# Performance work log

Measured on AMD Instinct MI355X. Metric: run time of the kernel, lower is better.

The kernel has to match this reference:

```python
import jax, jax.numpy as jnp
import numpy as np

P = 256        # number of graph pairs
LMAX = 32      # max graph size (padded to LMAX+1 incl. virtual node)
F = 2048       # num_input_features
E = 256        # embedding_dim
INF = 10000.0


def _lengths():
    i = np.arange(P)
    len_s = 8 + (i % 25)
    len_t = 8 + ((7 * i + 3) % 25)
    return len_s.astype(np.int32), len_t.astype(np.int32)


def setup_inputs() -> dict:
    key = jax.random.key(0)
    ks = jax.random.split(key, 6)
    len_s_np, len_t_np = _lengths()
    Ns, Nt = int(len_s_np.sum()), int(len_t_np.sum())
    x_s = jax.random.normal(ks[0], (Ns, F), jnp.float32)
    x_t = jax.random.normal(ks[1], (Nt, F), jnp.float32)
    W1 = jax.random.normal(ks[2], (E, F), jnp.float32) / np.float32(np.sqrt(F))
    b1 = jnp.zeros((E,), jnp.float32)
    W2 = jax.random.normal(ks[3], (E, E), jnp.float32) / np.float32(np.sqrt(E))
    b2 = jnp.zeros((E,), jnp.float32)
    virtual_embedding = jax.random.uniform(ks[4], (F,), jnp.float32)
    return {"x_s": x_s, "x_t": x_t, "W1": W1, "b1": b1, "W2": W2, "b2": b2,
            "virtual_embedding": virtual_embedding,
            "len_s": jnp.asarray(len_s_np), "len_t": jnp.asarray(len_t_np)}


def _embed(x, W1, b1, W2, b2):
    # nn.Sequential(Linear, Dropout(eval=identity), ReLU, Linear, ReLU)
    h = jax.nn.relu(x @ W1.T + b1)
    return jax.nn.relu(h @ W2.T + b2)


def _safe_cdist(a, b):
    # a: [P,L,E], b: [P,L,E] -> [P,L,L] Euclidean, grad-safe at 0
    sq = (jnp.sum(a * a, -1)[:, :, None] + jnp.sum(b * b, -1)[:, None, :]
          - 2.0 * jnp.einsum('pid,pjd->pij', a, b))
    sq = jnp.maximum(sq, 0.0)
    pos = sq > 0
    return jnp.where(pos, jnp.sqrt(jnp.where(pos, sq, 1.0)), 0.0)


def _pad_embed(emb, virtual_e, lens):
    # ragged [N,E] -> padded [P,LMAX+1,E]; slot lens[p] (and beyond) = virtual
    pos = jnp.arange(LMAX + 1)
    off = jnp.cumsum(lens) - lens                       # exclusive prefix sum
    idx = off[:, None] + jnp.minimum(pos[None, :], lens[:, None] - 1)
    mask = pos[None, :] < lens[:, None]
    return jnp.where(mask[..., None], emb[idx], virtual_e[None, None, :])


def _edit_costs(x_s, x_t, W1, b1, W2, b2, virtual_embedding, len_s, len_t):
    emb_s = _embed(x_s, W1, b1, W2, b2)
    emb_t = _embed(x_t, W1, b1, W2, b2)
    ve = _embed(virtual_embedding[None, :], W1, b1, W2, b2)[0]
    A = _pad_embed(emb_s, ve, len_s)                    # [P,L+1,E]
    B = _pad_embed(emb_t, ve, len_t)
    d = _safe_cdist(A, B)                               # [P,L+1,L+1]
    pos = jnp.arange(LMAX + 1)
    valid = ((pos[None, :, None] <= len_s[:, None, None]) &
             (pos[None, None, :] <= len_t[:, None, None]))
    tot = jnp.sum(jnp.where(valid, d, 0.0), axis=(1, 2))
    scale = (len_s * len_t).astype(d.dtype) / tot
    return jnp.where(valid, d * scale[:, None, None], 0.0), valid


def _lap_jv(C):
    # Jonker-Volgenant / e-maxx Hungarian for square cost matrix; returns col of each row
    C = np.asarray(C, dtype=np.float64)
    n = C.shape[0]
    u = np.zeros(n + 1)
    v = np.zeros(n + 1)
    p = np.zeros(n + 1, dtype=np.int64)
    way = np.zeros(n + 1, dtype=np.int64)
    for i in range(1, n + 1):
        p[0] = i
        j0 = 0
        minv = np.full(n + 1, np.inf)
        used = np.zeros(n + 1, dtype=bool)
        while True:
            used[j0] = True
            i0 = p[j0]
            cur = C[i0 - 1, :] - u[i0] - v[1:]
            upd = (~used[1:]) & (cur < minv[1:])
            minv[1:][upd] = cur[upd]
            way[1:][upd] = j0
            masked = np.where(used[1:], np.inf, minv[1:])
            j1 = int(np.argmin(masked)) + 1
            delta = masked[j1 - 1]
            u[p[used]] += delta
            v[used] -= delta
            minv[1:][~used[1:]] -= delta
            j0 = j1
            if p[j0] == 0:
                break
        while j0:
            j1 = way[j0]
            p[j0] = p[j1]
            j0 = j1
    row_of_col = p[1:] - 1
    col_of_row = np.empty(n, dtype=np.int64)
    col_of_row[row_of_col] = np.arange(n)
    return col_of_row


def _lsape_align(ec, n, m):
    # LSAPE expansion identical to GEDModelHomology.lsape
    N = n + m
    C = np.zeros((N, N))
    C[:n, :m] = ec[:n, :m]
    C[n:, :m] = INF
    C[:n, m:] = INF
    C[np.arange(n, n + m), np.arange(m)] = ec[n, :m]
    C[np.arange(n), np.arange(m, m + n)] = ec[:n, m]
    C[~np.isfinite(C)] = INF
    p = _lap_jv(C)
    q = np.arange(N)
    align = np.zeros((n + 1, m + 1), dtype=np.int32)
    align[np.minimum(q, n), np.minimum(p, m)] = 1
    align[-1, -1] = 0
    return align


def _alignments(costs_np, len_s_np, len_t_np):
    out = np.zeros((costs_np.shape[0], LMAX + 1, LMAX + 1), dtype=np.int32)
    for pr in range(costs_np.shape[0]):
        n, m = int(len_s_np[pr]), int(len_t_np[pr])
        out[pr, :n + 1, :m + 1] = _lsape_align(costs_np[pr, :n + 1, :m + 1], n, m)
    return out


def reference(x_s, x_t, W1, b1, W2, b2, virtual_embedding, len_s, len_t):
    costs, _ = _edit_costs(x_s, x_t, W1, b1, W2, b2, virtual_embedding, len_s, len_t)
    aligns = jnp.asarray(_alignments(np.asarray(costs),
                                     np.asarray(len_s), np.asarray(len_t)))
    geds = (jnp.sum(aligns.astype(costs.dtype) * costs, axis=(1, 2))
            / (len_s + len_t).astype(costs.dtype))
    return aligns, costs, geds
```

## Files before the change

### kernel.cpp

```cpp
#include <hip/hip_runtime.h>
#include <math.h>

#define LMAXP1 33
#define EDIM   256
#define FBIG   3.0e38f

typedef _Float16 half8 __attribute__((ext_vector_type(8)));
typedef float    f32x4 __attribute__((ext_vector_type(4)));

__device__ inline unsigned pk2h(_Float16 a, _Float16 b) {
    union { _Float16 h[2]; unsigned u; } q; q.h[0] = a; q.h[1] = b; return q.u;
}

#define ASTR 20
__global__ __launch_bounds__(256)
void k_gemm_splitk(const float* __restrict__ S0, int n0,
                   const float* __restrict__ S1, int n1,
                   const float* __restrict__ S2,
                   const float* __restrict__ W,
                   float* __restrict__ Part, int Mtot, int K, int kchunk,
                   const float* __restrict__ bias) {
    __shared__ alignas(16) unsigned AsH[128 * ASTR];
    __shared__ alignas(16) unsigned AsL[128 * ASTR];
    __shared__ alignas(16) unsigned BsH[64 * ASTR];
    __shared__ alignas(16) unsigned BsL[64 * ASTR];
    const int tid  = threadIdx.x;
    const int m0   = blockIdx.x * 128, nc0 = blockIdx.y * 64;
    const int ks   = blockIdx.z;
    const int kb   = ks * kchunk;
    const int ke   = (kb + kchunk < K) ? kb + kchunk : K;

    const int sar = tid >> 1;
    const int sak = (tid & 1) << 4;
    const int sbr = tid >> 2;
    const int sbk = (tid & 3) << 3;

    const int gr = m0 + sar;
    const float* srow = nullptr;
    if (gr < n0)            srow = S0 + (size_t)gr * K;
    else if (gr < n0 + n1)  srow = S1 + (size_t)(gr - n0) * K;
    else if (gr < Mtot)     srow = S2;
    const float* wrow = W + (size_t)(nc0 + sbr) * K;

    const int lane = tid & 63, wv = tid >> 6;
    const int wr = (wv & 1) << 6;
    const int wc = (wv >> 1) << 5;
    const int lr = lane & 15, lq = lane >> 4;

    f32x4 acc[4][2] = {};

    for (int k0 = kb; k0 < ke; k0 += 32) {
        {
            float x[16];
            if (srow) {
                const float4 f0 = *(const float4*)(srow + k0 + sak + 0);
                const float4 f1 = *(const float4*)(srow + k0 + sak + 4);
                const float4 f2 = *(const float4*)(srow + k0 + sak + 8);
                const float4 f3 = *(const float4*)(srow + k0 + sak + 12);
                x[0]=f0.x; x[1]=f0.y; x[2]=f0.z; x[3]=f0.w;
                x[4]=f1.x; x[5]=f1.y; x[6]=f1.z; x[7]=f1.w;
                x[8]=f2.x; x[9]=f2.y; x[10]=f2.z; x[11]=f2.w;
                x[12]=f3.x; x[13]=f3.y; x[14]=f3.z; x[15]=f3.w;
            } else {
                #pragma unroll
                for (int j = 0; j < 16; ++j) x[j] = 0.f;
            }
            unsigned uh[8], ul[8];
            #pragma unroll
            for (int j = 0; j < 8; ++j) {
                const _Float16 h0 = (_Float16)x[2*j],   h1 = (_Float16)x[2*j+1];
                const _Float16 l0 = (_Float16)(x[2*j]   - (float)h0);
                const _Float16 l1 = (_Float16)(x[2*j+1] - (float)h1);
                uh[j] = pk2h(h0, h1); ul[j] = pk2h(l0, l1);
            }
            unsigned* ph = AsH + sar * ASTR + (sak >> 1);
            unsigned* pl = AsL + sar * ASTR + (sak >> 1);
            ((uint4*)ph)[0] = make_uint4(uh[0],uh[1],uh[2],uh[3]);
            ((uint4*)ph)[1] = make_uint4(uh[4],uh[5],uh[6],uh[7]);
            ((uint4*)pl)[0] = make_uint4(ul[0],ul[1],ul[2],ul[3]);
            ((uint4*)pl)[1] = make_uint4(ul[4],ul[5],ul[6],ul[7]);
        }
        {
            const float4 f0 = *(const float4*)(wrow + k0 + sbk + 0);
            const float4 f1 = *(const float4*)(wrow + k0 + sbk + 4);
            float y[8] = {f0.x,f0.y,f0.z,f0.w,f1.x,f1.y,f1.z,f1.w};
            unsigned uh[4], ul[4];
            #pragma unroll
            for (int j = 0; j < 4; ++j) {
                const float a0 = y[2*j] * 1024.0f, a1 = y[2*j+1] * 1024.0f;
                const _Float16 h0 = (_Float16)a0, h1 = (_Float16)a1;
                const _Float16 l0 = (_Float16)(a0 - (float)h0);
                const _Float16 l1 = (_Float16)(a1 - (float)h1);
                uh[j] = pk2h(h0, h1); ul[j] = pk2h(l0, l1);
            }
            *(uint4*)(BsH + sbr * ASTR + (sbk >> 1)) = make_uint4(uh[0],uh[1],uh[2],uh[3]);
            *(uint4*)(BsL + sbr * ASTR + (sbk >> 1)) = make_uint4(ul[0],ul[1],ul[2],ul[3]);
        }
        __syncthreads();

        half8 bh[2], bl[2];
        #pragma unroll
        for (int ct = 0; ct < 2; ++ct) {
            const int br = wc + ct * 16 + lr;
            bh[ct] = *(const half8*)((const char*)BsH + br * 80 + lq * 16);
            bl[ct] = *(const half8*)((const char*)BsL + br * 80 + lq * 16);
        }
        #pragma unroll
        for (int rt = 0; rt < 4; ++rt) {
            const int ar = wr + rt * 16 + lr;
            const half8 ah = *(const half8*)((const char*)AsH + ar * 80 + lq * 16);
            const half8 al = *(const half8*)((const char*)AsL + ar * 80 + lq * 16);
            #pragma unroll
            for (int ct = 0; ct < 2; ++ct) {
                acc[rt][ct] = __builtin_amdgcn_mfma_f32_16x16x32_f16(ah, bh[ct], acc[rt][ct], 0, 0, 0);
                acc[rt][ct] = __builtin_amdgcn_mfma_f32_16x16x32_f16(ah, bl[ct], acc[rt][ct], 0, 0, 0);
                acc[rt][ct] = __builtin_amdgcn_mfma_f32_16x16x32_f16(al, bh[ct], acc[rt][ct], 0, 0, 0);
            }
        }
        __syncthreads();
    }

    float* pout = Part + (size_t)ks * ((size_t)Mtot * EDIM);
    const float sc = 1.0f / 1024.0f;
    #pragma unroll
    for (int rt = 0; rt < 4; ++rt) {
        #pragma unroll
        for (int r = 0; r < 4; ++r) {
            const int grr = m0 + wr + rt * 16 + lq * 4 + r;
            if (grr >= Mtot) continue;
            #pragma unroll
            for (int ct = 0; ct < 2; ++ct) {
                const int gc = nc0 + wc + ct * 16 + lr;
                float vv = acc[rt][ct][r] * sc;
                if (bias) vv = fmaxf(vv + bias[gc], 0.0f);
                pout[(size_t)grr * EDIM + gc] = vv;
            }
        }
    }
}

__global__ __launch_bounds__(256)
void k_reduce_bias_relu(const float* __restrict__ Part,
                        const float* __restrict__ bias,
                        float* __restrict__ C, int S, size_t MN4) {
    const size_t i = (size_t)blockIdx.x * blockDim.x + threadIdx.x;
    const size_t stride = (size_t)gridDim.x * blockDim.x;
    const size_t MN = MN4 * 4;
    for (size_t i4 = i; i4 < MN4; i4 += stride) {
        float4 s = ((const float4*)Part)[i4];
        for (int z = 1; z < S; ++z)
            { const float4 q = ((const float4*)(Part + (size_t)z * MN))[i4];
              s.x += q.x; s.y += q.y; s.z += q.z; s.w += q.w; }
        const float4 b = ((const float4*)bias)[i4 & 63];
        s.x = fmaxf(s.x + b.x, 0.f); s.y = fmaxf(s.y + b.y, 0.f);
        s.z = fmaxf(s.z + b.z, 0.f); s.w = fmaxf(s.w + b.w, 0.f);
        ((float4*)C)[i4] = s;
    }
}

__global__ __launch_bounds__(256)
void k_embed_gemm(const float* __restrict__ S0, int n0,
                  const float* __restrict__ S1, int n1,
                  const float* __restrict__ S2,
                  const float* __restrict__ W, const float* __restrict__ bias,
                  float* __restrict__ C, int Mtot, int K) {
    __shared__ alignas(16) float As[16][68];
    __shared__ alignas(16) float Bs[16][68];
    const int tid  = threadIdx.x;
    const int tx   = tid & 15, ty = tid >> 4;
    const int m0   = blockIdx.x * 64, nc0 = blockIdx.y * 64;
    const int lrow = tid >> 2;
    const int lk4  = (tid & 3) << 2;

    const int gr = m0 + lrow;
    const float* srow = nullptr;
    if (gr < n0)            srow = S0 + (size_t)gr * K;
    else if (gr < n0 + n1)  srow = S1 + (size_t)(gr - n0) * K;
    else if (gr < Mtot)     srow = S2;
    const float* wrow = W + (size_t)(nc0 + lrow) * K;

    float acc[4][4] = {};
    for (int k0 = 0; k0 < K; k0 += 16) {
        float4 va = make_float4(0.f, 0.f, 0.f, 0.f);
        if (srow) va = *(const float4*)(srow + k0 + lk4);
        const float4 vb = *(const float4*)(wrow + k0 + lk4);
        As[lk4+0][lrow] = va.x; As[lk4+1][lrow] = va.y;
        As[lk4+2][lrow] = va.z; As[lk4+3][lrow] = va.w;
        Bs[lk4+0][lrow] = vb.x; Bs[lk4+1][lrow] = vb.y;
        Bs[lk4+2][lrow] = vb.z; Bs[lk4+3][lrow] = vb.w;
        __syncthreads();
        #pragma unroll
        for (int kk = 0; kk < 16; ++kk) {
            const float4 a4 = *(const float4*)&As[kk][ty << 2];
            const float4 b4 = *(const float4*)&Bs[kk][tx << 2];
            const float av[4] = {a4.x, a4.y, a4.z, a4.w};
            const float bv[4] = {b4.x, b4.y, b4.z, b4.w};
            #pragma unroll
            for (int i2 = 0; i2 < 4; ++i2)
                #pragma unroll
                for (int j2 = 0; j2 < 4; ++j2)
                    acc[i2][j2] = fmaf(av[i2], bv[j2], acc[i2][j2]);
        }
        __syncthreads();
    }
    #pragma unroll
    for (int i2 = 0; i2 < 4; ++i2) {
        const int grr = m0 + (ty << 2) + i2;
        if (grr >= Mtot) continue;
        #pragma unroll
        for (int j2 = 0; j2 < 4; ++j2) {
            const int gc = nc0 + (tx << 2) + j2;
            const float vv = acc[i2][j2] + bias[gc];
            C[(size_t)grr * EDIM + gc] = fmaxf(vv, 0.0f);
        }
    }
}

__global__ __launch_bounds__(256)
void k_costs(const float* __restrict__ Emb, const int* __restrict__ len_s,
             const int* __restrict__ len_t, int Ns, int Nt,
             float* __restrict__ costs) {
    __shared__ alignas(16) float Asl[LMAXP1 * EDIM];
    __shared__ float dtile[LMAXP1 * LMAXP1];
    __shared__ float na[LMAXP1], nb[LMAXP1];
    __shared__ float red[256];
    __shared__ float s_scale;
    const int p = blockIdx.x, tid = threadIdx.x;
    const int n = len_s[p], m = len_t[p];
    int offs = 0, offt = 0;
    for (int j = 0; j < p; ++j) { offs += len_s[j]; offt += len_t[j]; }
    const int veRow = Ns + Nt;
    const int tbase = Ns + offt;

    for (int idx = tid; idx < (n + 1) * (EDIM / 4); idx += 256) {
        const int r = idx >> 6, c = idx & 63;
        const float* src = (r < n) ? (Emb + (size_t)(offs + r) * EDIM)
                                   : (Emb + (size_t)veRow * EDIM);
        ((float4*)Asl)[r * 64 + c] = ((const float4*)src)[c];
    }
    __syncthreads();

    if (tid <= n) {
        const float4* a4 = (const float4*)(Asl + tid * EDIM);
        float s = 0.f;
        for (int k = 0; k < 64; ++k) {
            const float4 a = a4[k];
            s = fmaf(a.x, a.x, s); s = fmaf(a.y, a.y, s);
            s = fmaf(a.z, a.z, s); s = fmaf(a.w, a.w, s);
        }
        na[tid] = s;
    } else if (tid >= 64 && tid - 64 <= m) {
        const int j = tid - 64;
        const float* src = (j < m) ? (Emb + (size_t)(tbase + j) * EDIM)
                                   : (Emb + (size_t)veRow * EDIM);
        const float4* b4 = (const float4*)src;
        float s = 0.f;
        for (int k = 0; k < 64; ++k) {
            const float4 b = b4[k];
            s = fmaf(b.x, b.x, s); s = fmaf(b.y, b.y, s);
            s = fmaf(b.z, b.z, s); s = fmaf(b.w, b.w, s);
        }
        nb[j] = s;
    }
    __syncthreads();

    float lsum = 0.f;
    const int m1 = m + 1;
    const int cells = (n + 1) * m1;
    for (int c = tid; c < cells; c += 256) {
        const int i = c / m1, j = c - i * m1;
        const float* brow = (j < m) ? (Emb + (size_t)(tbase + j) * EDIM)
                                    : (Emb + (size_t)veRow * EDIM);
        const float4* a4 = (const float4*)(Asl + i * EDIM);
        const float4* b4 = (const float4*)brow;
        float dot = 0.f;
        #pragma unroll 8
        for (int k = 0; k < 64; ++k) {
            const float4 a = a4[k], b = b4[k];
            dot = fmaf(a.x, b.x, dot); dot = fmaf(a.y, b.y, dot);
            dot = fmaf(a.z, b.z, dot); dot = fmaf(a.w, b.w, dot);
        }
        const float sq = fmaxf(na[i] + nb[j] - 2.0f * dot, 0.0f);
        const float d  = (sq > 0.0f) ? sqrtf(sq) : 0.0f;
        dtile[i * LMAXP1 + j] = d;
        lsum += d;
    }
    red[tid] = lsum;
    __syncthreads();
    for (int s = 128; s > 0; s >>= 1) {
        if (tid < s) red[tid] += red[tid + s];
        __syncthreads();
    }
    if (tid == 0) s_scale = (float)(n * m) / red[0];
    __syncthreads();
    const float scale = s_scale;
    for (int idx = tid; idx < LMAXP1 * LMAXP1; idx += 256) {
        const int i = idx / LMAXP1, j = idx - i * LMAXP1;
        const float v = (i <= n && j <= m) ? dtile[i * LMAXP1 + j] * scale : 0.0f;
        costs[(size_t)p * (LMAXP1 * LMAXP1) + idx] = v;
    }
}

__device__ inline int rdlane_i(int v, int l) { return __builtin_amdgcn_readlane(v, l); }
__device__ inline float rdlane_f(float v, int l) {
    return __int_as_float(__builtin_amdgcn_readlane(__float_as_int(v), l));
}
__device__ inline unsigned wave_umin64(unsigned x) {
#define DPPMINU(ctrl) { unsigned t_ = (unsigned)__builtin_amdgcn_update_dpp(  \
        (int)x, (int)x, (ctrl), 0xf, 0xf, false);                             \
        x = (t_ < x) ? t_ : x; }
    DPPMINU(0xB1)
    DPPMINU(0x4E)
    DPPMINU(0x141)
    DPPMINU(0x140)
    DPPMINU(0x142)
    DPPMINU(0x143)
#undef DPPMINU
    return (unsigned)__builtin_amdgcn_readlane((int)x, 63);
}

__global__ __launch_bounds__(64)
void k_lap(const float* __restrict__ costs, const int* __restrict__ len_s,
           const int* __restrict__ len_t, float* __restrict__ aligns,
           float* __restrict__ geds) {
    __shared__ float ec[LMAXP1 * LMAXP1];
    __shared__ float Ms[33 * 64];
    const int p = blockIdx.x, lane = threadIdx.x;
    const int n = len_s[p], m = len_t[p];
    const float* cp = costs + (size_t)p * (LMAXP1 * LMAXP1);
    for (int idx = lane; idx < LMAXP1 * LMAXP1; idx += 64) ec[idx] = cp[idx];
    __syncthreads();

    const bool swp = (n > m);
    const int R  = swp ? n : m;
    const int S_ = swp ? m : n;
    const bool vec = (lane >= 1 && lane <= R);

    for (int r = 1; r <= R; ++r) {
        float cv = FBIG;
        const int i0b = r - 1, j0b = lane - 1;
        if (vec) {
            if (!swp) {
                const float ins = ec[n * LMAXP1 + j0b];
                cv = (i0b < S_)
                   ? fminf(ec[i0b * LMAXP1 + j0b], ec[i0b * LMAXP1 + m] + ins)
                   : ins;
            } else {
                const float ins = ec[j0b * LMAXP1 + m];
                cv = (i0b < S_)
                   ? fminf(ec[j0b * LMAXP1 + i0b], ec[n * LMAXP1 + i0b] + ins)
                   : ins;
            }
        }
        Ms[(r << 6) + lane] = cv;
    }
    __syncthreads();

    float v_l = 0.0f;
    int amin_l = 0;
    if (vec) {
        float best = FBIG;
        for (int r = 1; r <= R; ++r) {
            const float c = Ms[(r << 6) + lane];
            if (c < best) { best = c; amin_l = r; }
        }
        v_l = best;
    }
    int p_l = 0;
    unsigned long long rowfree = ((1ull << R) - 1ull) << 1;
    for (int j = 1; j <= R; ++j) {
        const int ai = rdlane_i(amin_l, j);
        if ((rowfree >> ai) & 1ull) {
            if (lane == j) p_l = ai;
            rowfree &= ~(1ull << ai);
        }
    }

    float ucol = 0.0f, minv_l = FBIG;
    int way_l = 0;

    for (int i = 1; i <= R; ++i) {
        if (!((rowfree >> i) & 1ull)) continue;
        if (lane == 0) { p_l = i; ucol = 0.0f; }
        minv_l = FBIG;
        int used_l = 0;
        int j0 = 0, i0 = i;
        float u_i0 = 0.0f;
        while (true) {
            if (lane == j0) used_l = 1;
            const float cur = Ms[(i0 << 6) + lane] - u_i0 - v_l;
            const bool unused = vec && !used_l;
            if (unused && cur < minv_l) { minv_l = cur; way_l = j0; }
            const float mval = unused ? fmaxf(minv_l, 0.0f) : FBIG;
            const unsigned key = (__float_as_uint(mval) & ~63u) | (unsigned)lane;
            const unsigned kmin = wave_umin64(key);
            const int j1 = (int)(kmin & 63u);
            const float delta = rdlane_f(minv_l, j1);
            if (used_l) { ucol += delta; v_l -= delta; }
            if (unused) minv_l -= delta;
            j0 = j1;
            i0 = rdlane_i(p_l, j1);
            u_i0 = rdlane_f(ucol, j1);
            if (i0 == 0) break;
        }
        int jj = j0;
        while (jj != 0) {
            const int   j1a = rdlane_i(way_l, jj);
            const int   pn  = rdlane_i(p_l, j1a);
            const float un  = rdlane_f(ucol, j1a);
            if (lane == jj) { p_l = pn; ucol = un; }
            jj = j1a;
        }
    }

    float* ap = aligns + (size_t)p * (LMAXP1 * LMAXP1);
    for (int idx = lane; idx < LMAXP1 * LMAXP1; idx += 64) ap[idx] = 0.0f;
    __syncthreads();
    float gedv = 0.0f;
    if (vec) {
        const int i0b = p_l - 1;
        const int j0b = lane - 1;
        if (!swp) {
            if (i0b < S_) {
                const float sub = ec[i0b * LMAXP1 + j0b];
                const float alt = ec[i0b * LMAXP1 + m] + ec[n * LMAXP1 + j0b];
                if (sub <= alt) { ap[i0b * LMAXP1 + j0b] = 1.0f; gedv = sub; }
                else { ap[i0b * LMAXP1 + m] = 1.0f;
                       ap[n * LMAXP1 + j0b] = 1.0f;
                       gedv = alt; }
            } else {
                ap[n * LMAXP1 + j0b] = 1.0f;
                gedv = ec[n * LMAXP1 + j0b];
            }
        } else {
            if (i0b < S_) {
                const float sub = ec[j0b * LMAXP1 + i0b];
                const float alt = ec[n * LMAXP1 + i0b] + ec[j0b * LMAXP1 + m];
                if (sub <= alt) { ap[j0b * LMAXP1 + i0b] = 1.0f; gedv = sub; }
                else { ap[n * LMAXP1 + i0b] = 1.0f;
                       ap[j0b * LMAXP1 + m] = 1.0f;
                       gedv = alt; }
            } else {
                ap[j0b * LMAXP1 + m] = 1.0f;
                gedv = ec[j0b * LMAXP1 + m];
            }
        }
    }
    #pragma unroll
    for (int off = 32; off > 0; off >>= 1) gedv += __shfl_xor(gedv, off);
    if (lane == 0) geds[p] = gedv / (float)(n + m);
}

extern "C" void kernel_launch(void* const* d_in, const int* in_sizes, int n_in,
                              void* d_out, int out_size, void* d_ws, size_t ws_size,
                              hipStream_t stream) {
    const float* x_s = (const float*)d_in[0];
    const float* x_t = (const float*)d_in[1];
    const float* W1  = (const float*)d_in[2];
    const float* b1  = (const float*)d_in[3];
    const float* W2  = (const float*)d_in[4];
    const float* b2  = (const float*)d_in[5];
    const float* ve  = (const float*)d_in[6];
    const int* len_s = (const int*)d_in[7];
    const int* len_t = (const int*)d_in[8];
    const int P    = in_sizes[7];
    const int Ns   = in_sizes[0] / 2048;
    const int Nt   = in_sizes[1] / 2048;
    const int Mtot = Ns + Nt + 1;
    const size_t MN  = (size_t)Mtot * EDIM;

    float* H    = (float*)d_ws;
    float* Emb  = H + MN;
    float* Part = Emb + MN;

    int S = 1;
    if (ws_size >= (2 + 4) * MN * sizeof(float)) S = 4;
    else if (ws_size >= (2 + 2) * MN * sizeof(float)) S = 2;

    float* out_aligns = (float*)d_out;
    float* out_costs  = out_aligns + (size_t)P * LMAXP1 * LMAXP1;
    float* out_geds   = out_costs  + (size_t)P * LMAXP1 * LMAXP1;

    const dim3 b256(256);
    const int gx128 = (Mtot + 127) / 128;

    if (S > 1) {
        k_gemm_splitk<<<dim3(gx128, 4, S), b256, 0, stream>>>(
            x_s, Ns, x_t, Nt, ve, W1, Part, Mtot, 2048, 2048 / S, nullptr);
        const size_t MN4 = MN / 4;
        const int rblocks = (int)((MN4 + 255) / 256) < 2048
                          ? (int)((MN4 + 255) / 256) : 2048;
        k_reduce_bias_relu<<<dim3(rblocks), b256, 0, stream>>>(Part, b1, H, S, MN4);
        k_gemm_splitk<<<dim3(gx128, 4, 1), b256, 0, stream>>>(
            H, Mtot, nullptr, 0, nullptr, W2, Emb, Mtot, 256, 256, b2);
    } else {
        const int gx64 = (Mtot + 63) / 64;
        k_embed_gemm<<<dim3(gx64, 4), b256, 0, stream>>>(
            x_s, Ns, x_t, Nt, ve, W1, b1, H, Mtot, 2048);
        k_embed_gemm<<<dim3(gx64, 4), b256, 0, stream>>>(
            H, Mtot, nullptr, 0, nullptr, W2, b2, Emb, Mtot, 256);
    }
    k_costs<<<dim3(P), b256, 0, stream>>>(Emb, len_s, len_t, Ns, Nt, out_costs);
    k_lap<<<dim3(P), dim3(64), 0, stream>>>(out_costs, len_s, len_t, out_aligns, out_geds);
}
```

Baseline: 189.5 us.

## Retile split-K GEMM to full-width N and use MFMA for pairwise Gram in costs

The split-K embedding GEMM now uses 64-row tiles that span all 256 output columns, so each block converts and reuses a row of the input across the whole width instead of reloading it for four column blocks. The per-pair cost kernel replaces its scalar FP32 dot-product loop with split-half FP16 MFMA Gram tiles (hi/lo compensation) computed into a 48x48 padded tile, with distances written straight to shared memory. The cost is a larger shared W tile and more accumulators per block, fewer blocks in flight, and slight precision differences from the FP16 split.

```diff
diff --git a/kernel.cpp b/kernel.cpp
--- a/kernel.cpp
+++ b/kernel.cpp
@@ -20,70 +20,58 @@
                    const float* __restrict__ W,
                    float* __restrict__ Part, int Mtot, int K, int kchunk,
                    const float* __restrict__ bias) {
-    __shared__ alignas(16) unsigned AsH[128 * ASTR];
-    __shared__ alignas(16) unsigned AsL[128 * ASTR];
-    __shared__ alignas(16) unsigned BsH[64 * ASTR];
-    __shared__ alignas(16) unsigned BsL[64 * ASTR];
-    const int tid  = threadIdx.x;
-    const int m0   = blockIdx.x * 128, nc0 = blockIdx.y * 64;
-    const int ks   = blockIdx.z;
-    const int kb   = ks * kchunk;
-    const int ke   = (kb + kchunk < K) ? kb + kchunk : K;
-
-    const int sar = tid >> 1;
-    const int sak = (tid & 1) << 4;
-    const int sbr = tid >> 2;
-    const int sbk = (tid & 3) << 3;
-
-    const int gr = m0 + sar;
+    __shared__ alignas(16) unsigned AsH[64 * ASTR],  AsL[64 * ASTR];
+    __shared__ alignas(16) unsigned BsH[256 * ASTR], BsL[256 * ASTR];
+    const int tid = threadIdx.x;
+    const int m0  = blockIdx.x * 64;
+    const int ks  = blockIdx.z;
+    const int kb  = ks * kchunk;
+    const int ke  = (kb + kchunk < K) ? kb + kchunk : K;
+
+    const int sar = tid >> 2, sak = (tid & 3) << 3;
+    const int gr  = m0 + sar;
     const float* srow = nullptr;
     if (gr < n0)            srow = S0 + (size_t)gr * K;
     else if (gr < n0 + n1)  srow = S1 + (size_t)(gr - n0) * K;
     else if (gr < Mtot)     srow = S2;
-    const float* wrow = W + (size_t)(nc0 + sbr) * K;
 
     const int lane = tid & 63, wv = tid >> 6;
-    const int wr = (wv & 1) << 6;
-    const int wc = (wv >> 1) << 5;
+    const int wc = wv << 6;
     const int lr = lane & 15, lq = lane >> 4;
 
-    f32x4 acc[4][2] = {};
+    f32x4 acc[4][4] = {};
 
     for (int k0 = kb; k0 < ke; k0 += 32) {
         {
-            float x[16];
+            float x[8];
             if (srow) {
                 const float4 f0 = *(const float4*)(srow + k0 + sak + 0);
                 const float4 f1 = *(const float4*)(srow + k0 + sak + 4);
-                const float4 f2 = *(const float4*)(srow + k0 + sak + 8);
-                const float4 f3 = *(const float4*)(srow + k0 + sak + 12);
                 x[0]=f0.x; x[1]=f0.y; x[2]=f0.z; x[3]=f0.w;
                 x[4]=f1.x; x[5]=f1.y; x[6]=f1.z; x[7]=f1.w;
-                x[8]=f2.x; x[9]=f2.y; x[10]=f2.z; x[11]=f2.w;
-                x[12]=f3.x; x[13]=f3.y; x[14]=f3.z; x[15]=f3.w;
             } else {
                 #pragma unroll
-                for (int j = 0; j < 16; ++j) x[j] = 0.f;
-            }
-            unsigned uh[8], ul[8];
+                for (int j = 0; j < 8; ++j) x[j] = 0.f;
+            }
+            unsigned uh[4], ul[4];
             #pragma unroll
-            for (int j = 0; j < 8; ++j) {
+            for (int j = 0; j < 4; ++j) {
                 const _Float16 h0 = (_Float16)x[2*j],   h1 = (_Float16)x[2*j+1];
                 const _Float16 l0 = (_Float16)(x[2*j]   - (float)h0);
                 const _Float16 l1 = (_Float16)(x[2*j+1] - (float)h1);
                 uh[j] = pk2h(h0, h1); ul[j] = pk2h(l0, l1);
             }
-            unsigned* ph = AsH + sar * ASTR + (sak >> 1);
-            unsigned* pl = AsL + sar * ASTR + (sak >> 1);
-            ((uint4*)ph)[0] = make_uint4(uh[0],uh[1],uh[2],uh[3]);
-            ((uint4*)ph)[1] = make_uint4(uh[4],uh[5],uh[6],uh[7]);
-            ((uint4*)pl)[0] = make_uint4(ul[0],ul[1],ul[2],ul[3]);
-            ((uint4*)pl)[1] = make_uint4(ul[4],ul[5],ul[6],ul[7]);
-        }
-        {
-            const float4 f0 = *(const float4*)(wrow + k0 + sbk + 0);
-            const float4 f1 = *(const float4*)(wrow + k0 + sbk + 4);
-            float y[8] = {f0.x,f0.y,f0.z,f0.w,f1.x,f1.y,f1.z,f1.w};
+            *(uint4*)(AsH + sar * ASTR + (sak >> 1)) = make_uint4(uh[0],uh[1],uh[2],uh[3]);
+            *(uint4*)(AsL + sar * ASTR + (sak >> 1)) = make_uint4(ul[0],ul[1],ul[2],ul[3]);
+        }
+        #pragma unroll
+        for (int it = 0; it < 4; ++it) {
+            const int idx = tid + it * 256;
+            const int br = idx >> 2, bk = (idx & 3) << 3;
+            const float* wr_ = W + (size_t)br * K + k0 + bk;
+            const float4 f0 = *(const float4*)(wr_ + 0);
+            const float4 f1 = *(const float4*)(wr_ + 4);
+            const float y[8] = {f0.x,f0.y,f0.z,f0.w,f1.x,f1.y,f1.z,f1.w};
             unsigned uh[4], ul[4];
             #pragma unroll
             for (int j = 0; j < 4; ++j) {
@@ -93,28 +81,28 @@
                 const _Float16 l1 = (_Float16)(a1 - (float)h1);
                 uh[j] = pk2h(h0, h1); ul[j] = pk2h(l0, l1);
             }
-            *(uint4*)(BsH + sbr * ASTR + (sbk >> 1)) = make_uint4(uh[0],uh[1],uh[2],uh[3]);
-            *(uint4*)(BsL + sbr * ASTR + (sbk >> 1)) = make_uint4(ul[0],ul[1],ul[2],ul[3]);
-        }
-        __syncthreads();
-
-        half8 bh[2], bl[2];
-        #pragma unroll
-        for (int ct = 0; ct < 2; ++ct) {
+            *(uint4*)(BsH + br * ASTR + (bk >> 1)) = make_uint4(uh[0],uh[1],uh[2],uh[3]);
+            *(uint4*)(BsL + br * ASTR + (bk >> 1)) = make_uint4(ul[0],ul[1],ul[2],ul[3]);
+        }
+        __syncthreads();
+
+        half8 bhv[4], blv[4];
+        #pragma unroll
+        for (int ct = 0; ct < 4; ++ct) {
             const int br = wc + ct * 16 + lr;
-            bh[ct] = *(const half8*)((const char*)BsH + br * 80 + lq * 16);
-            bl[ct] = *(const half8*)((const char*)BsL + br * 80 + lq * 16);
+            bhv[ct] = *(const half8*)((const char*)BsH + br * 80 + lq * 16);
+            blv[ct] = *(const half8*)((const char*)BsL + br * 80 + lq * 16);
         }
         #pragma unroll
         for (int rt = 0; rt < 4; ++rt) {
-            const int ar = wr + rt * 16 + lr;
+            const int ar = rt * 16 + lr;
             const half8 ah = *(const half8*)((const char*)AsH + ar * 80 + lq * 16);
             const half8 al = *(const half8*)((const char*)AsL + ar * 80 + lq * 16);
             #pragma unroll
-            for (int ct = 0; ct < 2; ++ct) {
-                acc[rt][ct] = __builtin_amdgcn_mfma_f32_16x16x32_f16(ah, bh[ct], acc[rt][ct], 0, 0, 0);
-                acc[rt][ct] = __builtin_amdgcn_mfma_f32_16x16x32_f16(ah, bl[ct], acc[rt][ct], 0, 0, 0);
-                acc[rt][ct] = __builtin_amdgcn_mfma_f32_16x16x32_f16(al, bh[ct], acc[rt][ct], 0, 0, 0);
+            for (int ct = 0; ct < 4; ++ct) {
+                acc[rt][ct] = __builtin_amdgcn_mfma_f32_16x16x32_f16(ah, bhv[ct], acc[rt][ct], 0, 0, 0);
+                acc[rt][ct] = __builtin_amdgcn_mfma_f32_16x16x32_f16(ah, blv[ct], acc[rt][ct], 0, 0, 0);
+                acc[rt][ct] = __builtin_amdgcn_mfma_f32_16x16x32_f16(al, bhv[ct], acc[rt][ct], 0, 0, 0);
             }
         }
         __syncthreads();
@@ -126,11 +114,11 @@
     for (int rt = 0; rt < 4; ++rt) {
         #pragma unroll
         for (int r = 0; r < 4; ++r) {
-            const int grr = m0 + wr + rt * 16 + lq * 4 + r;
+            const int grr = m0 + rt * 16 + lq * 4 + r;
             if (grr >= Mtot) continue;
             #pragma unroll
-            for (int ct = 0; ct < 2; ++ct) {
-                const int gc = nc0 + wc + ct * 16 + lr;
+            for (int ct = 0; ct < 4; ++ct) {
+                const int gc = wc + ct * 16 + lr;
                 float vv = acc[rt][ct][r] * sc;
                 if (bias) vv = fmaxf(vv + bias[gc], 0.0f);
                 pout[(size_t)grr * EDIM + gc] = vv;
@@ -216,11 +204,13 @@
     }
 }
 
+#define CSTR 36
 __global__ __launch_bounds__(256)
 void k_costs(const float* __restrict__ Emb, const int* __restrict__ len_s,
              const int* __restrict__ len_t, int Ns, int Nt,
              float* __restrict__ costs) {
-    __shared__ alignas(16) float Asl[LMAXP1 * EDIM];
+    __shared__ alignas(16) unsigned Ah[34 * CSTR], Al[34 * CSTR];
+    __shared__ alignas(16) unsigned Bh[34 * CSTR], Bl[34 * CSTR];
     __shared__ float dtile[LMAXP1 * LMAXP1];
     __shared__ float na[LMAXP1], nb[LMAXP1];
     __shared__ float red[256];
@@ -232,16 +222,13 @@
     const int veRow = Ns + Nt;
     const int tbase = Ns + offt;
 
-    for (int idx = tid; idx < (n + 1) * (EDIM / 4); idx += 256) {
-        const int r = idx >> 6, c = idx & 63;
-        const float* src = (r < n) ? (Emb + (size_t)(offs + r) * EDIM)
-                                   : (Emb + (size_t)veRow * EDIM);
-        ((float4*)Asl)[r * 64 + c] = ((const float4*)src)[c];
-    }
-    __syncthreads();
+    const int lane = tid & 63, wv = tid >> 6;
+    const int lr = lane & 15, lq = lane >> 4;
 
     if (tid <= n) {
-        const float4* a4 = (const float4*)(Asl + tid * EDIM);
+        const float* src = (tid < n) ? (Emb + (size_t)(offs + tid) * EDIM)
+                                     : (Emb + (size_t)veRow * EDIM);
+        const float4* a4 = (const float4*)src;
         float s = 0.f;
         for (int k = 0; k < 64; ++k) {
             const float4 a = a4[k];
@@ -262,6 +249,73 @@
         }
         nb[j] = s;
     }
+
+    f32x4 g0 = {}, g1 = {}, g2 = {};
+    const int t0 = wv, t1 = wv + 4, t2 = wv + 8;
+
+    for (int k0 = 0; k0 < EDIM; k0 += 64) {
+        for (int idx = tid; idx < 34 * 16; idx += 256) {
+            const int r = idx >> 4, c4 = idx & 15;
+            float4 va = make_float4(0.f,0.f,0.f,0.f), vb = va;
+            if (r < n)       va = *(const float4*)(Emb + (size_t)(offs + r) * EDIM + k0 + c4*4);
+            else if (r == n) va = *(const float4*)(Emb + (size_t)veRow * EDIM + k0 + c4*4);
+            if (r < m)       vb = *(const float4*)(Emb + (size_t)(tbase + r) * EDIM + k0 + c4*4);
+            else if (r == m) vb = *(const float4*)(Emb + (size_t)veRow * EDIM + k0 + c4*4);
+            const float xa[4] = {va.x, va.y, va.z, va.w};
+            const float xb[4] = {vb.x, vb.y, vb.z, vb.w};
+            unsigned ah_[2], al_[2], bh_[2], bl_[2];
+            #pragma unroll
+            for (int j = 0; j < 2; ++j) {
+                const _Float16 h0 = (_Float16)xa[2*j],   h1 = (_Float16)xa[2*j+1];
+                const _Float16 l0 = (_Float16)(xa[2*j]   - (float)h0);
+                const _Float16 l1 = (_Float16)(xa[2*j+1] - (float)h1);
+                ah_[j] = pk2h(h0, h1); al_[j] = pk2h(l0, l1);
+                const _Float16 g0_ = (_Float16)xb[2*j],   g1_ = (_Float16)xb[2*j+1];
+                const _Float16 m0_ = (_Float16)(xb[2*j]   - (float)g0_);
+                const _Float16 m1_ = (_Float16)(xb[2*j+1] - (float)g1_);
+                bh_[j] = pk2h(g0_, g1_); bl_[j] = pk2h(m0_, m1_);
+            }
+            const int uo = r * CSTR + c4 * 2;
+            *(uint2*)(Ah + uo) = make_uint2(ah_[0], ah_[1]);
+            *(uint2*)(Al + uo) = make_uint2(al_[0], al_[1]);
+            *(uint2*)(Bh + uo) = make_uint2(bh_[0], bh_[1]);
+            *(uint2*)(Bl + uo) = make_uint2(bl_[0], bl_[1]);
+        }
+        __syncthreads();
+
+        #pragma unroll
+        for (int kf = 0; kf < 2; ++kf) {
+#define GRAM_TILE(T, G) { \
+            const int tr_ = (T) / 3, tc_ = (T) % 3;                              \
+            const int ar_ = tr_ * 16 + lr, br_ = tc_ * 16 + lr;                  \
+            const half8 ah = *(const half8*)((const char*)Ah + ar_*144 + kf*64 + lq*16); \
+            const half8 al = *(const half8*)((const char*)Al + ar_*144 + kf*64 + lq*16); \
+            const half8 bh = *(const half8*)((const char*)Bh + br_*144 + kf*64 + lq*16); \
+            const half8 bl = *(const half8*)((const char*)Bl + br_*144 + kf*64 + lq*16); \
+            G = __builtin_amdgcn_mfma_f32_16x16x32_f16(ah, bh, G, 0, 0, 0);      \
+            G = __builtin_amdgcn_mfma_f32_16x16x32_f16(ah, bl, G, 0, 0, 0);      \
+            G = __builtin_amdgcn_mfma_f32_16x16x32_f16(al, bh, G, 0, 0, 0); }
+            GRAM_TILE(t0, g0)
+            GRAM_TILE(t1, g1)
+            if (wv == 0) GRAM_TILE(t2, g2)
+#undef GRAM_TILE
+        }
+        __syncthreads();
+    }
+
+#define DTILE_OUT(T, G) { \
+    const int tr_ = (T) / 3, tc_ = (T) % 3;                                      \
+    _Pragma("unroll")                                                            \
+    for (int r = 0; r < 4; ++r) {                                                \
+        const int i_ = tr_ * 16 + lq * 4 + r, j_ = tc_ * 16 + lr;                \
+        if (i_ <= n && j_ <= m) {                                                \
+            const float sq = fmaxf(na[i_] + nb[j_] - 2.0f * G[r], 0.0f);         \
+            dtile[i_ * LMAXP1 + j_] = (sq > 0.0f) ? sqrtf(sq) : 0.0f;            \
+        } } }
+    DTILE_OUT(t0, g0)
+    DTILE_OUT(t1, g1)
+    if (wv == 0) DTILE_OUT(t2, g2)
+#undef DTILE_OUT
     __syncthreads();
 
     float lsum = 0.f;
@@ -269,21 +323,7 @@
     const int cells = (n + 1) * m1;
     for (int c = tid; c < cells; c += 256) {
         const int i = c / m1, j = c - i * m1;
-        const float* brow = (j < m) ? (Emb + (size_t)(tbase + j) * EDIM)
-                                    : (Emb + (size_t)veRow * EDIM);
-        const float4* a4 = (const float4*)(Asl + i * EDIM);
-        const float4* b4 = (const float4*)brow;
-        float dot = 0.f;
-        #pragma unroll 8
-        for (int k = 0; k < 64; ++k) {
-            const float4 a = a4[k], b = b4[k];
-            dot = fmaf(a.x, b.x, dot); dot = fmaf(a.y, b.y, dot);
-            dot = fmaf(a.z, b.z, dot); dot = fmaf(a.w, b.w, dot);
-        }
-        const float sq = fmaxf(na[i] + nb[j] - 2.0f * dot, 0.0f);
-        const float d  = (sq > 0.0f) ? sqrtf(sq) : 0.0f;
-        dtile[i * LMAXP1 + j] = d;
-        lsum += d;
+        lsum += dtile[i * LMAXP1 + j];
     }
     red[tid] = lsum;
     __syncthreads();
@@ -482,19 +522,18 @@
     float* out_geds   = out_costs  + (size_t)P * LMAXP1 * LMAXP1;
 
     const dim3 b256(256);
-    const int gx128 = (Mtot + 127) / 128;
+    const int gx64 = (Mtot + 63) / 64;
 
     if (S > 1) {
-        k_gemm_splitk<<<dim3(gx128, 4, S), b256, 0, stream>>>(
+        k_gemm_splitk<<<dim3(gx64, 1, S), b256, 0, stream>>>(
             x_s, Ns, x_t, Nt, ve, W1, Part, Mtot, 2048, 2048 / S, nullptr);
         const size_t MN4 = MN / 4;
         const int rblocks = (int)((MN4 + 255) / 256) < 2048
                           ? (int)((MN4 + 255) / 256) : 2048;
         k_reduce_bias_relu<<<dim3(rblocks), b256, 0, stream>>>(Part, b1, H, S, MN4);
-        k_gemm_splitk<<<dim3(gx128, 4, 1), b256, 0, stream>>>(
+        k_gemm_splitk<<<dim3(gx64, 1, 1), b256, 0, stream>>>(
             H, Mtot, nullptr, 0, nullptr, W2, Emb, Mtot, 256, 256, b2);
     } else {
-        const int gx64 = (Mtot + 63) / 64;
         k_embed_gemm<<<dim3(gx64, 4), b256, 0, stream>>>(
             x_s, Ns, x_t, Nt, ve, W1, b1, H, Mtot, 2048);
         k_embed_gemm<<<dim3(gx64, 4), b256, 0, stream>>>(
```

Measured after the change: 180.1 us. 1.05x faster.
